# Kernel optimization log

Hardware: AMD Instinct MI355X
Metric: run time of the kernel (lower is better)

## Reference

```python
import jax, jax.numpy as jnp
import numpy as np

GAMMA = 2.0
ALPHA = 0.25
NEG_TH = 0.4
POS_TH = 0.5
NUM_CLASSES = 80
STRIDES = [8, 16, 32, 64, 128]
IMG_H, IMG_W = 800, 1024
LEVEL_HW = [(100, 128), (50, 64), (25, 32), (13, 16), (7, 8)]


def _base_anchors(stride):
    # standard RetinaNet: octave_base_scale=4, 3 scales/octave, ratios 0.5/1/2
    scales = 4.0 * stride * np.array([2 ** 0, 2 ** (1.0 / 3), 2 ** (2.0 / 3)])
    ratios = np.array([0.5, 1.0, 2.0])
    h_r = np.sqrt(ratios)
    w_r = 1.0 / h_r
    ws = (w_r[:, None] * scales[None, :]).reshape(-1)
    hs = (h_r[:, None] * scales[None, :]).reshape(-1)
    return np.stack([-ws / 2, -hs / 2, ws / 2, hs / 2], axis=1)  # [9,4]


def build_anchors():
    out = []
    for (h, w), s in zip(LEVEL_HW, STRIDES):
        base = _base_anchors(s)
        xs = (np.arange(w) + 0.5) * s
        ys = (np.arange(h) + 0.5) * s
        cx, cy = np.meshgrid(xs, ys)  # [h,w]
        ctr = np.stack([cx, cy, cx, cy], axis=-1)  # [h,w,4]
        a = ctr[:, :, None, :] + base[None, None, :, :]  # [h,w,9,4] anchor-fastest
        out.append(a.reshape(-1, 4))
    return jnp.asarray(np.concatenate(out, axis=0), dtype=jnp.float32)  # [A,4]


def _iou(gt, an):  # [G,4],[A,4] -> [G,A]
    lt = jnp.maximum(gt[:, None, :2], an[None, :, :2])
    rb = jnp.minimum(gt[:, None, 2:], an[None, :, 2:])
    wh = jnp.clip(rb - lt, 0.0)
    inter = wh[..., 0] * wh[..., 1]
    area_g = (gt[:, 2] - gt[:, 0]) * (gt[:, 3] - gt[:, 1])
    area_a = (an[:, 2] - an[:, 0]) * (an[:, 3] - an[:, 1])
    return inter / (area_g[:, None] + area_a[None, :] - inter + 1e-6)


def _encode(an, gt):  # delta encoding, mean=0 std=1
    aw = an[:, 2] - an[:, 0]
    ah = an[:, 3] - an[:, 1]
    ax = (an[:, 0] + an[:, 2]) * 0.5
    ay = (an[:, 1] + an[:, 3]) * 0.5
    gw = gt[:, 2] - gt[:, 0]
    gh = gt[:, 3] - gt[:, 1]
    gx = (gt[:, 0] + gt[:, 2]) * 0.5
    gy = (gt[:, 1] + gt[:, 3]) * 0.5
    return jnp.stack([(gx - ax) / aw, (gy - ay) / ah, jnp.log(gw / aw), jnp.log(gh / ah)], axis=1)


def _per_image(logits, regp, gtb, gtl, anchors):
    G = gtb.shape[0]
    iou = _iou(gtb, anchors)  # [G,A]
    max_ov = iou.max(axis=0)
    arg_ov = iou.argmax(axis=0)
    assigned = jnp.where(max_ov < NEG_TH, 0, -1)
    assigned = jnp.where(max_ov >= POS_TH, arg_ov + 1, assigned)
    max_gt = iou.max(axis=1)
    eq = iou == max_gt[:, None]
    any_eq = eq.any(axis=0)
    last_j = (G - 1) - jnp.argmax(eq[::-1], axis=0)
    assigned = jnp.where(any_eq, last_j + 1, assigned)
    pos = assigned > 0
    neg = assigned == 0
    gi = jnp.clip(assigned - 1, 0, G - 1)
    labels = jnp.where(pos, gtl[gi], NUM_CLASSES)  # negatives get label = num_classes
    include = (pos | neg).astype(logits.dtype)  # ignored anchors contribute 0
    # focal loss
    p = jnp.clip(jax.nn.sigmoid(logits), 1e-6, 1.0 - 1e-6)
    cr = jnp.arange(NUM_CLASSES)[None, :]
    t = labels[:, None]
    term1 = (1.0 - p) ** GAMMA * jnp.log(p)
    term2 = p ** GAMMA * jnp.log(1.0 - p)
    per = -(t == cr).astype(p.dtype) * term1 * ALPHA - ((t != cr) & (t >= 0)).astype(p.dtype) * term2 * (1.0 - ALPHA)
    cls_sum = (per.sum(axis=1) * include).sum()
    # smooth-free L1 on positives
    reg_t = _encode(anchors, gtb[gi])
    reg_sum = (jnp.abs(regp - reg_t).sum(axis=1) * pos.astype(regp.dtype)).sum()
    return cls_sum, reg_sum, pos.sum()


def _flatten_levels(levels, c):
    n = levels[0].shape[0]
    return jnp.concatenate([p.transpose(0, 2, 3, 1).reshape(n, -1, c) for p in levels], axis=1)


def reference(cls_p0, cls_p1, cls_p2, cls_p3, cls_p4, reg_p0, reg_p1, reg_p2, reg_p3, reg_p4, gt_bboxes, gt_labels):
    anchors = build_anchors()
    cls = _flatten_levels([cls_p0, cls_p1, cls_p2, cls_p3, cls_p4], NUM_CLASSES)  # [N,A,80]
    reg = _flatten_levels([reg_p0, reg_p1, reg_p2, reg_p3, reg_p4], 4)  # [N,A,4]
    cls_s, reg_s, npos = jax.vmap(lambda l, r, b, t: _per_image(l, r, b, t, anchors))(cls, reg, gt_bboxes, gt_labels)
    num_pos = jnp.maximum(npos.sum(), 1).astype(cls.dtype)
    return (cls_s.sum() / num_pos, reg_s.sum() / num_pos)


def setup_inputs() -> dict:
    key = jax.random.key(0)
    ks = jax.random.split(key, 16)
    N, G = 2, 32
    d = {}
    for i, (h, w) in enumerate(LEVEL_HW):
        d[f"cls_p{i}"] = jax.random.normal(ks[i], (N, 9 * NUM_CLASSES, h, w), jnp.float32)
        d[f"reg_p{i}"] = jax.random.normal(ks[5 + i], (N, 9 * 4, h, w), jnp.float32)
    cx = jax.random.uniform(ks[10], (N, G), minval=50.0, maxval=IMG_W - 50.0)
    cy = jax.random.uniform(ks[11], (N, G), minval=50.0, maxval=IMG_H - 50.0)
    bw = jax.random.uniform(ks[12], (N, G), minval=32.0, maxval=300.0)
    bh = jax.random.uniform(ks[13], (N, G), minval=32.0, maxval=300.0)
    x1 = jnp.clip(cx - bw / 2, 0.0, IMG_W - 2.0)
    y1 = jnp.clip(cy - bh / 2, 0.0, IMG_H - 2.0)
    x2 = jnp.clip(cx + bw / 2, x1 + 1.0, float(IMG_W))
    y2 = jnp.clip(cy + bh / 2, y1 + 1.0, float(IMG_H))
    d["gt_bboxes"] = jnp.stack([x1, y1, x2, y2], axis=-1)
    d["gt_labels"] = jax.random.randint(ks[14], (N, G), 0, NUM_CLASSES)
    return d
```

## Files before the change

### kernel.cpp

```cpp
#include <hip/hip_runtime.h>
#include <stdint.h>

namespace {
constexpr int A_TOTAL = 153576;
constexpr int NG      = 32;
constexpr int NIMG    = 2;
constexpr int NCLS    = 80;
constexpr int NBLK_CLS = 9720;

constexpr size_t WS_CLS0  = 0;
constexpr size_t WS_REG   = 2048;
constexpr size_t WS_NPOS  = 2056;
constexpr size_t WS_MAXGT = 2112;
constexpr size_t WS_LABEL = 2560;
constexpr size_t WS_ZERO  = 2560;
}

__device__ __attribute__((noinline)) float4 anchor_box(int idx) {
    int base, lw, stride;
    if      (idx < 115200) { base = 0;      lw = 7; stride = 8;   }
    else if (idx < 144000) { base = 115200; lw = 6; stride = 16;  }
    else if (idx < 151200) { base = 144000; lw = 5; stride = 32;  }
    else if (idx < 153072) { base = 151200; lw = 4; stride = 64;  }
    else                   { base = 153072; lw = 3; stride = 128; }
    int s    = idx - base;
    int cell = s / 9;
    int a    = s - cell * 9;
    int y    = cell >> lw;
    int x    = cell - (y << lw);
    int r    = a / 3;
    int k    = a - r * 3;
    double c3 = (k == 0) ? 1.0 : ((k == 1) ? 1.2599210498948731648 : 1.5874010519681994748);
    double hr = (r == 0) ? 0.70710678118654752440 : ((r == 1) ? 1.0 : 1.4142135623730950488);
    double scale = 4.0 * (double)stride * c3;
    double wr  = 1.0 / hr;
    double wsz = wr * scale;
    double hsz = hr * scale;
    double cx  = ((double)x + 0.5) * (double)stride;
    double cy  = ((double)y + 0.5) * (double)stride;
    float4 out;
    out.x = (float)(cx - wsz / 2.0);
    out.y = (float)(cy - hsz / 2.0);
    out.z = (float)(cx + wsz / 2.0);
    out.w = (float)(cy + hsz / 2.0);
    return out;
}

__device__ __attribute__((noinline)) float iou_fn(float4 an, float4 g) {
    float ltx = fmaxf(g.x, an.x), lty = fmaxf(g.y, an.y);
    float rbx = fminf(g.z, an.z), rby = fminf(g.w, an.w);
    float w = fmaxf(rbx - ltx, 0.f), h = fmaxf(rby - lty, 0.f);
    float inter = w * h;
    float ag = (g.z - g.x) * (g.w - g.y);
    float aa = (an.z - an.x) * (an.w - an.y);
    return inter / (ag + aa - inter + 1e-6f);
}

__global__ __launch_bounds__(256)
void kmaxgt(const float* __restrict__ gtb, unsigned* __restrict__ maxgt) {
    int n   = blockIdx.y;
    int tid = threadIdx.x;
    int anchor = blockIdx.x * 256 + tid;
    __shared__ float4   g_s[NG];
    __shared__ unsigned smax[NG];
    if (tid < NG) {
        g_s[tid]  = ((const float4*)gtb)[n * NG + tid];
        smax[tid] = 0u;
    }
    __syncthreads();
    bool  valid = anchor < A_TOTAL;
    float4 an = anchor_box(valid ? anchor : 0);
    int lane = tid & 63;
    for (int j = 0; j < NG; ++j) {
        float iou = valid ? iou_fn(an, g_s[j]) : 0.f;
        for (int off = 32; off; off >>= 1)
            iou = fmaxf(iou, __shfl_xor(iou, off));
        if (lane == 0) atomicMax(&smax[j], __float_as_uint(iou));
    }
    __syncthreads();
    if (tid < NG) atomicMax(&maxgt[n * NG + tid], smax[tid]);
}

__global__ __launch_bounds__(256)
void kassign(const float* __restrict__ gtb, const int* __restrict__ gtl,
             const float* __restrict__ maxgt, uint8_t* __restrict__ labels,
             const float* __restrict__ r0, const float* __restrict__ r1,
             const float* __restrict__ r2, const float* __restrict__ r3,
             const float* __restrict__ r4,
             double* __restrict__ reg_acc, int* __restrict__ npos_acc) {
    int n   = blockIdx.y;
    int tid = threadIdx.x;
    int anchor = blockIdx.x * 256 + tid;
    __shared__ float4 g_s[NG];
    __shared__ float  mg_s[NG];
    __shared__ int    gl_s[NG];
    if (tid < NG) {
        g_s[tid]  = ((const float4*)gtb)[n * NG + tid];
        mg_s[tid] = maxgt[n * NG + tid];
        gl_s[tid] = gtl[n * NG + tid];
    }
    __syncthreads();
    bool  valid = anchor < A_TOTAL;
    float4 an = anchor_box(valid ? anchor : 0);
    float best = -1.f; int arg = 0; int last = -1;
    for (int j = 0; j < NG; ++j) {
        float iou = iou_fn(an, g_s[j]);
        if (iou > best) { best = iou; arg = j; }
        if (iou == mg_s[j]) last = j;
    }
    int assigned = -1;
    if (best < 0.4f)  assigned = 0;
    if (best >= 0.5f) assigned = arg + 1;
    if (last >= 0)    assigned = last + 1;

    float rsum = 0.f; bool pos = false;
    if (valid) {
        int base, HW; const float* rp;
        if      (anchor < 115200) { base = 0;      HW = 12800; rp = r0; }
        else if (anchor < 144000) { base = 115200; HW = 3200;  rp = r1; }
        else if (anchor < 151200) { base = 144000; HW = 800;   rp = r2; }
        else if (anchor < 153072) { base = 151200; HW = 208;   rp = r3; }
        else                      { base = 153072; HW = 56;    rp = r4; }
        int s = anchor - base;
        int cell = s / 9; int a = s - cell * 9;

        uint8_t lab;
        if (assigned > 0) {
            pos = true;
            int gi = assigned - 1;
            lab = (uint8_t)gl_s[gi];
            float aw = an.z - an.x, ah = an.w - an.y;
            float ax = (an.x + an.z) * 0.5f, ay = (an.y + an.w) * 0.5f;
            float4 g = g_s[gi];
            float gw = g.z - g.x, gh = g.w - g.y;
            float gx = (g.x + g.z) * 0.5f, gy = (g.y + g.w) * 0.5f;
            float t0 = (gx - ax) / aw, t1 = (gy - ay) / ah;
            float t2 = __logf(gw / aw), t3 = __logf(gh / ah);
            long off = (long)(n * 36 + a * 4) * HW + cell;
            float p0 = rp[off], p1 = rp[off + HW], p2 = rp[off + 2 * HW], p3 = rp[off + 3 * HW];
            rsum = fabsf(p0 - t0) + fabsf(p1 - t1) + fabsf(p2 - t2) + fabsf(p3 - t3);
        } else {
            lab = (assigned == 0) ? (uint8_t)NCLS : (uint8_t)255;
        }
        labels[n * A_TOTAL + base + a * HW + cell] = lab;
    }
    for (int off = 32; off; off >>= 1) rsum += __shfl_xor(rsum, off);
    unsigned long long bal = __ballot(pos);
    __shared__ float pr[4];
    __shared__ int   pn[4];
    int wid = tid >> 6;
    if ((tid & 63) == 0) { pr[wid] = rsum; pn[wid] = __popcll(bal); }
    __syncthreads();
    if (tid == 0) {
        float s = pr[0] + pr[1] + pr[2] + pr[3];
        int   c = pn[0] + pn[1] + pn[2] + pn[3];
        atomicAdd(reg_acc, (double)s);
        atomicAdd(npos_acc, c);
    }
}

__device__ __forceinline__ float focal(float z, int c, int lab) {
    float e   = __expf(z);
    float u   = 1.f + e;
    float inv = __builtin_amdgcn_rcpf(u);
    float L   = __logf(u);
    float p   = e * inv;
    float t2  = 0.75f * (p * p) * L;
    float t1  = 0.25f * (inv * inv) * (L - z);
    float r   = (c == lab) ? t1 : t2;
    return (lab == 255) ? 0.f : r;
}

template <int HW, int BASE, int BPL>
__device__ float cls_level(const float* __restrict__ cp,
                           const uint8_t* __restrict__ labels, int rel) {
    int slab  = rel / (BPL * 4);
    int rem   = rel - slab * (BPL * 4);
    int chunk = rem >> 2;
    int cq    = rem & 3;
    int n = slab / 9, a = slab - 9 * n;
    int cell = chunk * 128 + 2 * (int)threadIdx.x;
    if (cell >= HW) return 0.f;
    int lb = n * A_TOTAL + BASE + a * HW + cell;
    int lab0 = labels[lb], lab1 = labels[lb + 1];
    const float* p = cp + (size_t)(n * 720 + a * 80 + cq * 20) * HW + cell;
    int cbase = cq * 20;
    float acc = 0.f;
#pragma unroll 10
    for (int c = 0; c < 20; ++c, p += HW) {
        float2 z = *(const float2*)p;
        acc += focal(z.x, cbase + c, lab0);
        acc += focal(z.y, cbase + c, lab1);
    }
    return acc;
}

__global__ __launch_bounds__(64)
void kcls(const float* __restrict__ c0, const float* __restrict__ c1,
          const float* __restrict__ c2, const float* __restrict__ c3,
          const float* __restrict__ c4,
          const uint8_t* __restrict__ labels, char* __restrict__ ws) {
    int b = blockIdx.x;
    float v;
    if      (b < 7200) v = cls_level<12800, 0,      100>(c0, labels, b);
    else if (b < 9000) v = cls_level<3200,  115200, 25 >(c1, labels, b - 7200);
    else if (b < 9504) v = cls_level<800,   144000, 7  >(c2, labels, b - 9000);
    else if (b < 9648) v = cls_level<208,   151200, 2  >(c3, labels, b - 9504);
    else               v = cls_level<56,    153072, 1  >(c4, labels, b - 9648);
    for (int off = 32; off; off >>= 1) v += __shfl_xor(v, off);
    if (threadIdx.x == 0)
        atomicAdd((double*)(ws + WS_CLS0 + (size_t)(b & 7) * 256), (double)v);
}

__global__ void kfinal(const char* __restrict__ ws, float* __restrict__ out) {
    double cls = 0.0;
    for (int i = 0; i < 8; ++i) cls += *(const double*)(ws + WS_CLS0 + (size_t)i * 256);
    double reg = *(const double*)(ws + WS_REG);
    int    np  = *(const int*)(ws + WS_NPOS);
    float denom = (float)(np > 1 ? np : 1);
    out[0] = (float)cls / denom;
    out[1] = (float)reg / denom;
}

extern "C" void kernel_launch(void* const* d_in, const int* in_sizes, int n_in,
                              void* d_out, int out_size, void* d_ws, size_t ws_size,
                              hipStream_t stream) {
    static const int HWs[5] = {12800, 3200, 800, 208, 56};
    const float* cls_p[5] = {nullptr, nullptr, nullptr, nullptr, nullptr};
    const float* reg_p[5] = {nullptr, nullptr, nullptr, nullptr, nullptr};
    const float* gtb = nullptr;
    const int*   gtl = nullptr;
    for (int i = 0; i < n_in; ++i) {
        int sz = in_sizes[i];
        if (sz == NIMG * NG * 4) { gtb = (const float*)d_in[i]; continue; }
        if (sz == NIMG * NG)     { gtl = (const int*)d_in[i];   continue; }
        for (int l = 0; l < 5; ++l) {
            if (sz == NIMG * 9 * NCLS * HWs[l]) { cls_p[l] = (const float*)d_in[i]; break; }
            if (sz == NIMG * 9 * 4 * HWs[l])    { reg_p[l] = (const float*)d_in[i]; break; }
        }
    }
    float* out = (float*)d_out;

    char* ws = (char*)d_ws;
    hipMemsetAsync(d_ws, 0, WS_ZERO, stream);
    unsigned* maxgt_u = (unsigned*)(ws + WS_MAXGT);
    float*    maxgt_f = (float*)(ws + WS_MAXGT);
    uint8_t*  labels  = (uint8_t*)(ws + WS_LABEL);
    double*   reg_acc = (double*)(ws + WS_REG);
    int*      npos    = (int*)(ws + WS_NPOS);

    dim3 gAB((A_TOTAL + 255) / 256, NIMG);
    kmaxgt<<<gAB, 256, 0, stream>>>(gtb, maxgt_u);
    kassign<<<gAB, 256, 0, stream>>>(gtb, gtl, maxgt_f, labels,
                                     reg_p[0], reg_p[1], reg_p[2], reg_p[3], reg_p[4],
                                     reg_acc, npos);
    kcls<<<NBLK_CLS, 64, 0, stream>>>(cls_p[0], cls_p[1], cls_p[2], cls_p[3], cls_p[4],
                                      labels, ws);
    kfinal<<<1, 1, 0, stream>>>(ws, out);
}
```

Baseline: 216.4 us.

## Split GT loop across thread pairs and spread reg/npos atomics over slots

kmaxgt and kassign now assign two threads per anchor, each handling 16 of the 32 ground-truth boxes, and combine their partial max/argmax/last results with lane shuffles. This doubles the number of blocks, to shorten per-thread serial IoU work and raise parallelism. The regression-loss and positive-count atomics are spread over 8 padded slots, which kfinal sums, to reduce contention on a single address. The cost is recomputing the anchor box in both threads of a pair and idling half the threads during the regression part.

```diff
diff --git a/kernel.cpp b/kernel.cpp
--- a/kernel.cpp
+++ b/kernel.cpp
@@ -10,10 +10,10 @@
 
 constexpr size_t WS_CLS0  = 0;
 constexpr size_t WS_REG   = 2048;
-constexpr size_t WS_NPOS  = 2056;
-constexpr size_t WS_MAXGT = 2112;
-constexpr size_t WS_LABEL = 2560;
-constexpr size_t WS_ZERO  = 2560;
+constexpr size_t WS_NPOS  = 4096;
+constexpr size_t WS_MAXGT = 6144;
+constexpr size_t WS_LABEL = 6656;
+constexpr size_t WS_ZERO  = 6656;
 }
 
 __device__ __attribute__((noinline)) float4 anchor_box(int idx) {
@@ -60,7 +60,8 @@
 void kmaxgt(const float* __restrict__ gtb, unsigned* __restrict__ maxgt) {
     int n   = blockIdx.y;
     int tid = threadIdx.x;
-    int anchor = blockIdx.x * 256 + tid;
+    int anchor = blockIdx.x * 128 + (tid >> 1);
+    int half   = tid & 1;
     __shared__ float4   g_s[NG];
     __shared__ unsigned smax[NG];
     if (tid < NG) {
@@ -71,11 +72,12 @@
     bool  valid = anchor < A_TOTAL;
     float4 an = anchor_box(valid ? anchor : 0);
     int lane = tid & 63;
-    for (int j = 0; j < NG; ++j) {
+    for (int jj = 0; jj < 16; ++jj) {
+        int j = half * 16 + jj;
         float iou = valid ? iou_fn(an, g_s[j]) : 0.f;
-        for (int off = 32; off; off >>= 1)
+        for (int off = 2; off <= 32; off <<= 1)
             iou = fmaxf(iou, __shfl_xor(iou, off));
-        if (lane == 0) atomicMax(&smax[j], __float_as_uint(iou));
+        if (lane < 2) atomicMax(&smax[j], __float_as_uint(iou));
     }
     __syncthreads();
     if (tid < NG) atomicMax(&maxgt[n * NG + tid], smax[tid]);
@@ -87,10 +89,11 @@
              const float* __restrict__ r0, const float* __restrict__ r1,
              const float* __restrict__ r2, const float* __restrict__ r3,
              const float* __restrict__ r4,
-             double* __restrict__ reg_acc, int* __restrict__ npos_acc) {
+             char* __restrict__ ws) {
     int n   = blockIdx.y;
     int tid = threadIdx.x;
-    int anchor = blockIdx.x * 256 + tid;
+    int anchor = blockIdx.x * 128 + (tid >> 1);
+    int half   = tid & 1;
     __shared__ float4 g_s[NG];
     __shared__ float  mg_s[NG];
     __shared__ int    gl_s[NG];
@@ -103,18 +106,24 @@
     bool  valid = anchor < A_TOTAL;
     float4 an = anchor_box(valid ? anchor : 0);
     float best = -1.f; int arg = 0; int last = -1;
-    for (int j = 0; j < NG; ++j) {
+    for (int jj = 0; jj < 16; ++jj) {
+        int j = half * 16 + jj;
         float iou = iou_fn(an, g_s[j]);
         if (iou > best) { best = iou; arg = j; }
         if (iou == mg_s[j]) last = j;
     }
+    float ob = __shfl_xor(best, 1);
+    int   oa = __shfl_xor(arg, 1);
+    int   ol = __shfl_xor(last, 1);
+    if (ob > best) { best = ob; arg = oa; }
+    if (ol > last) last = ol;
     int assigned = -1;
     if (best < 0.4f)  assigned = 0;
     if (best >= 0.5f) assigned = arg + 1;
     if (last >= 0)    assigned = last + 1;
 
     float rsum = 0.f; bool pos = false;
-    if (valid) {
+    if (valid && half == 0) {
         int base, HW; const float* rp;
         if      (anchor < 115200) { base = 0;      HW = 12800; rp = r0; }
         else if (anchor < 144000) { base = 115200; HW = 3200;  rp = r1; }
@@ -154,8 +163,9 @@
     if (tid == 0) {
         float s = pr[0] + pr[1] + pr[2] + pr[3];
         int   c = pn[0] + pn[1] + pn[2] + pn[3];
-        atomicAdd(reg_acc, (double)s);
-        atomicAdd(npos_acc, c);
+        size_t slot = (size_t)(blockIdx.x & 7) * 256;
+        atomicAdd((double*)(ws + WS_REG  + slot), (double)s);
+        atomicAdd((int*)   (ws + WS_NPOS + slot), c);
     }
 }
 
@@ -213,10 +223,13 @@
 }
 
 __global__ void kfinal(const char* __restrict__ ws, float* __restrict__ out) {
-    double cls = 0.0;
-    for (int i = 0; i < 8; ++i) cls += *(const double*)(ws + WS_CLS0 + (size_t)i * 256);
-    double reg = *(const double*)(ws + WS_REG);
-    int    np  = *(const int*)(ws + WS_NPOS);
+    double cls = 0.0, reg = 0.0;
+    int np = 0;
+    for (int i = 0; i < 8; ++i) {
+        cls += *(const double*)(ws + WS_CLS0 + (size_t)i * 256);
+        reg += *(const double*)(ws + WS_REG  + (size_t)i * 256);
+        np  += *(const int*)   (ws + WS_NPOS + (size_t)i * 256);
+    }
     float denom = (float)(np > 1 ? np : 1);
     out[0] = (float)cls / denom;
     out[1] = (float)reg / denom;
@@ -246,14 +259,12 @@
     unsigned* maxgt_u = (unsigned*)(ws + WS_MAXGT);
     float*    maxgt_f = (float*)(ws + WS_MAXGT);
     uint8_t*  labels  = (uint8_t*)(ws + WS_LABEL);
-    double*   reg_acc = (double*)(ws + WS_REG);
-    int*      npos    = (int*)(ws + WS_NPOS);
-
-    dim3 gAB((A_TOTAL + 255) / 256, NIMG);
+
+    dim3 gAB((A_TOTAL + 127) / 128, NIMG);
     kmaxgt<<<gAB, 256, 0, stream>>>(gtb, maxgt_u);
     kassign<<<gAB, 256, 0, stream>>>(gtb, gtl, maxgt_f, labels,
                                      reg_p[0], reg_p[1], reg_p[2], reg_p[3], reg_p[4],
-                                     reg_acc, npos);
+                                     ws);
     kcls<<<NBLK_CLS, 64, 0, stream>>>(cls_p[0], cls_p[1], cls_p[2], cls_p[3], cls_p[4],
                                       labels, ws);
     kfinal<<<1, 1, 0, stream>>>(ws, out);
```

Result: faster. 194.4 us (-10.2%).
